# Optimization experiments

Measured on AMD Instinct MI355X. Metric: run time of the kernel, lower is better.

The kernel has to match this reference:

```python
import jax, jax.numpy as jnp
import numpy as np
from jax import lax

B, L, C = 8, 2048, 512
CR = C // 4      # SE reduction hidden
DH = C // 2      # fusion d_hidden
KS = [3, 7, 15, 20]
EPS = 1e-5


def _ln(x, g, b):
    m = jnp.mean(x, -1, keepdims=True)
    v = jnp.mean((x - m) ** 2, -1, keepdims=True)
    return (x - m) / jnp.sqrt(v + EPS) * g + b


def _bn(x, g, b, m, v):  # x: [B,C,L], eval-mode BatchNorm1d
    return (x - m[:, None]) / jnp.sqrt(v[:, None] + EPS) * g[:, None] + b[:, None]


def _forward(x, pw_w, pw_b, pw_bn_g, pw_bn_b, pw_bn_m, pw_bn_v,
             dw_w0, dw_w1, dw_w2, dw_w3, dw_b, dw_bn_g, dw_bn_b, dw_bn_m, dw_bn_v,
             se_w1, se_b1, se_w2, se_b2, se_ln_g, se_ln_b,
             df_ln_g, df_ln_b, wq, bq, wv, bv, wg, bg,
             op_w, op_b, op_ln_g, op_ln_b, fn_g, fn_b):
    Bs, Ls, Cs = x.shape
    x_in = jnp.transpose(x, (0, 2, 1))                      # [B,C,L]
    # pointwise conv (1x1) + BN + ReLU
    x_pw = jnp.einsum('oc,bcl->bol', pw_w, x_in) + pw_b[:, None]
    x_pw = jax.nn.relu(_bn(x_pw, pw_bn_g, pw_bn_b, pw_bn_m, pw_bn_v))

    enhanced = []
    for i, (w, k) in enumerate(zip([dw_w0, dw_w1, dw_w2, dw_w3], KS)):
        p = (k - 1) // 2
        y = lax.conv_general_dilated(
            x_pw, w[:, None, :], window_strides=(1,), padding=[(p, p)],
            feature_group_count=Cs, dimension_numbers=('NCH', 'OIH', 'NCH'))
        y = y + dw_b[i][:, None]
        y = jax.nn.relu(_bn(y, dw_bn_g[i], dw_bn_b[i], dw_bn_m[i], dw_bn_v[i]))
        if y.shape[2] > Ls:
            y = y[:, :, :Ls]
        elif y.shape[2] < Ls:
            y = jnp.pad(y, ((0, 0), (0, 0), (0, Ls - y.shape[2])))
        feat = jnp.transpose(y, (0, 2, 1))                  # [B,L,C]
        # ChannelAttentionBlock (SE): pool over L -> MLP -> sigmoid gate -> residual LN
        ym = jnp.mean(feat, axis=1)                          # [B,C]
        h = jax.nn.relu(ym @ se_w1[i].T + se_b1[i])          # [B,CR]
        wt = jax.nn.sigmoid(h @ se_w2[i].T + se_b2[i])       # [B,C]
        enhanced.append(_ln(feat + feat * wt[:, None, :], se_ln_g[i], se_ln_b[i]))

    # diff_conv: fixed weight w[:,:,0]=-1, w[:,:,1]=1 => every out channel is
    # sum_c(x[l+1,c]-x[l,c]); pad one zero step at the end
    s = jnp.sum(x[:, 1:] - x[:, :-1], axis=-1, keepdims=True)    # [B,L-1,1]
    diff_feat = jnp.pad(jnp.broadcast_to(s, (Bs, Ls - 1, Cs)), ((0, 0), (0, 1), (0, 0)))

    # DiffGuidedInteractiveFusion
    D = _ln(diff_feat, df_ln_g, df_ln_b)
    Q = D @ wq.T + bq                                       # [B,L,DH]
    scores = []
    for f in enhanced:
        Vi = f @ wv.T + bv                                  # [B,L,DH]
        scores.append(jnp.tanh(Q * Vi) @ wg + bg)           # [B,L]
    scores = jnp.stack(scores, axis=-1)                     # [B,L,S]
    sw = jax.nn.softmax(scores, axis=-1)
    fused = sum(sw[..., i:i + 1] * enhanced[i] for i in range(len(enhanced)))
    out = _ln(fused @ op_w.T + op_b, op_ln_g, op_ln_b)
    return _ln(out + x, fn_g, fn_b)


def setup_inputs() -> dict:
    key = jax.random.key(0)
    ks = jax.random.split(key, 12)
    r = lambda k, s: jax.random.normal(k, s, jnp.float32) * 0.02
    return {
        'x': jax.random.normal(ks[0], (B, L, C), jnp.float32),
        'pw_w': r(ks[1], (C, C)), 'pw_b': jnp.zeros(C),
        'pw_bn_g': jnp.ones(C), 'pw_bn_b': jnp.zeros(C), 'pw_bn_m': jnp.zeros(C), 'pw_bn_v': jnp.ones(C),
        'dw_w0': r(ks[2], (C, 3)), 'dw_w1': r(ks[3], (C, 7)), 'dw_w2': r(ks[4], (C, 15)), 'dw_w3': r(ks[5], (C, 20)),
        'dw_b': jnp.zeros((4, C)),
        'dw_bn_g': jnp.ones((4, C)), 'dw_bn_b': jnp.zeros((4, C)), 'dw_bn_m': jnp.zeros((4, C)), 'dw_bn_v': jnp.ones((4, C)),
        'se_w1': r(ks[6], (4, CR, C)), 'se_b1': jnp.zeros((4, CR)),
        'se_w2': r(ks[7], (4, C, CR)), 'se_b2': jnp.zeros((4, C)),
        'se_ln_g': jnp.ones((4, C)), 'se_ln_b': jnp.zeros((4, C)),
        'df_ln_g': jnp.ones(C), 'df_ln_b': jnp.zeros(C),
        'wq': r(ks[8], (DH, C)), 'bq': jnp.zeros(DH),
        'wv': r(ks[9], (DH, C)), 'bv': jnp.zeros(DH),
        'wg': r(ks[10], (DH,)), 'bg': jnp.zeros(()),
        'op_w': r(ks[11], (C, C)), 'op_b': jnp.zeros(C),
        'op_ln_g': jnp.ones(C), 'op_ln_b': jnp.zeros(C),
        'fn_g': jnp.ones(C), 'fn_b': jnp.zeros(C),
    }


def reference(x, pw_w, pw_b, pw_bn_g, pw_bn_b, pw_bn_m, pw_bn_v,
              dw_w0, dw_w1, dw_w2, dw_w3, dw_b, dw_bn_g, dw_bn_b, dw_bn_m, dw_bn_v,
              se_w1, se_b1, se_w2, se_b2, se_ln_g, se_ln_b,
              df_ln_g, df_ln_b, wq, bq, wv, bv, wg, bg,
              op_w, op_b, op_ln_g, op_ln_b, fn_g, fn_b):
    return _forward(x, pw_w, pw_b, pw_bn_g, pw_bn_b, pw_bn_m, pw_bn_v,
                    dw_w0, dw_w1, dw_w2, dw_w3, dw_b, dw_bn_g, dw_bn_b, dw_bn_m, dw_bn_v,
                    se_w1, se_b1, se_w2, se_b2, se_ln_g, se_ln_b,
                    df_ln_g, df_ln_b, wq, bq, wv, bv, wg, bg,
                    op_w, op_b, op_ln_g, op_ln_b, fn_g, fn_b)
```

## Files before the change

kernel.cpp:

```cpp
#include <hip/hip_runtime.h>
#include <math.h>

static constexpr int Bz = 8;
static constexpr int Lz = 2048;
static constexpr int Cz = 512;
static constexpr int CRz = 128;
static constexpr int DHz = 256;
static constexpr int MT = Bz * Lz;
static constexpr float EPSz = 1e-5f;

typedef unsigned short u16;
typedef __bf16 bf16x8 __attribute__((ext_vector_type(8)));
typedef float f32x4 __attribute__((ext_vector_type(4)));
typedef unsigned short u16x8 __attribute__((ext_vector_type(8)));

__device__ __forceinline__ float bf2f(u16 u) {
  unsigned int v = ((unsigned int)u) << 16;
  return __builtin_bit_cast(float, v);
}
__device__ __forceinline__ u16 f2bf(float f) {
  unsigned int b = __builtin_bit_cast(unsigned int, f);
  b += 0x7FFFu + ((b >> 16) & 1u);
  return (u16)(b >> 16);
}
__device__ __forceinline__ f32x4 mfma16(bf16x8 a, bf16x8 b, f32x4 c) {
  return __builtin_amdgcn_mfma_f32_16x16x32_bf16(a, b, c, 0, 0, 0);
}

__global__ __launch_bounds__(256) void cvt_bf16_kernel(
    const float* __restrict__ src, u16* __restrict__ dst, int n8) {
  int i = blockIdx.x * 256 + threadIdx.x;
  if (i >= n8) return;
  const float4* s = (const float4*)src;
  float4 a = s[i * 2], b = s[i * 2 + 1];
  u16x8 o;
  o[0] = f2bf(a.x); o[1] = f2bf(a.y); o[2] = f2bf(a.z); o[3] = f2bf(a.w);
  o[4] = f2bf(b.x); o[5] = f2bf(b.y); o[6] = f2bf(b.z); o[7] = f2bf(b.w);
  ((u16x8*)dst)[i] = o;
}

__global__ __launch_bounds__(256) void prep_kernel(
    const float* __restrict__ pw_b, const float* __restrict__ pw_g,
    const float* __restrict__ pw_bb, const float* __restrict__ pw_m,
    const float* __restrict__ pw_v,
    const float* __restrict__ dw_b, const float* __restrict__ dw_g,
    const float* __restrict__ dw_bb, const float* __restrict__ dw_m,
    const float* __restrict__ dw_v,
    const float* __restrict__ df_ln_b, const float* __restrict__ wq,
    const float* __restrict__ bq,
    float* __restrict__ pwA, float* __restrict__ pwB,
    float* __restrict__ dwA, float* __restrict__ dwB,
    float* __restrict__ qc) {
  const int blk = blockIdx.x;
  const int t = threadIdx.x;
  if (blk == 0) {
    for (int c = t; c < Cz; c += 256) {
      float inv = rsqrtf(pw_v[c] + EPSz);
      float a = pw_g[c] * inv;
      float bb = pw_bb[c] - pw_m[c] * a;
      pwA[c] = a;
      pwB[c] = pw_b[c] * a + bb;
    }
  } else if (blk <= 4) {
    const int i = blk - 1;
    for (int c = t; c < Cz; c += 256) {
      int idx = i * Cz + c;
      float inv = rsqrtf(dw_v[idx] + EPSz);
      float a = dw_g[idx] * inv;
      float bb = dw_bb[idx] - dw_m[idx] * a;
      dwA[idx] = a;
      dwB[idx] = dw_b[idx] * a + bb;
    }
  } else {
    if (t < DHz) {
      float s = bq[t];
      const float* w = wq + (size_t)t * Cz;
      for (int c = 0; c < Cz; c++) s += df_ln_b[c] * w[c];
      qc[t] = s;
    }
  }
}

__global__ __launch_bounds__(256, 2) void pw_mfma_kernel(
    const u16* __restrict__ Wbf, const float* __restrict__ x,
    const float* __restrict__ alpha, const float* __restrict__ beta,
    u16* __restrict__ xpw) {
  __shared__ __align__(16) char lds[74240];
  u16(*sX)[520] = (u16(*)[520])lds;
  u16(*sW)[40] = (u16(*)[40])(lds + 33280);
  u16* sC = (u16*)(lds + 33280);
  __shared__ float sAl[Cz];
  __shared__ float sBe[Cz];
  const int bat = blockIdx.x >> 6;
  const int l0 = (blockIdx.x & 63) * 32;
  const int t = threadIdx.x;
  const int lane = t & 63, w = t >> 6;
  const int fr = lane & 15, fk = (lane >> 4) * 8;
  const int mh = (w >> 1) * 16;
  const int nh = (w & 1) * 16;
#pragma unroll
  for (int rep = 0; rep < 8; rep++) {
    const int idx = rep * 256 + t;
    const int row = idx >> 6;
    const int col = (idx & 63) * 8;
    const float* src = x + ((size_t)bat * Lz + l0 + row) * Cz + col;
    float4 f0 = *(const float4*)src;
    float4 f1 = *(const float4*)(src + 4);
    u16x8 o;
    o[0] = f2bf(f0.x); o[1] = f2bf(f0.y); o[2] = f2bf(f0.z); o[3] = f2bf(f0.w);
    o[4] = f2bf(f1.x); o[5] = f2bf(f1.y); o[6] = f2bf(f1.z); o[7] = f2bf(f1.w);
    *(u16x8*)&sX[row][col] = o;
  }
  for (int c = t; c < Cz; c += 256) { sAl[c] = alpha[c]; sBe[c] = beta[c]; }
  f32x4 acc[16];
#pragma unroll
  for (int mf = 0; mf < 16; mf++)
#pragma unroll
    for (int r = 0; r < 4; r++) acc[mf][r] = 0.f;
  const int wrow = t >> 2, wch = (t & 3) * 8;
  const u16* wbase = Wbf + (size_t)wrow * Cz + wch;
  u16x8 breg[8];
#pragma unroll
  for (int rep = 0; rep < 8; rep++)
    breg[rep] = *(const u16x8*)(wbase + (size_t)rep * 64 * Cz);
  for (int k0 = 0; k0 < Cz; k0 += 32) {
    __syncthreads();
#pragma unroll
    for (int rep = 0; rep < 8; rep++)
      *(u16x8*)&sW[rep * 64 + wrow][wch] = breg[rep];
    __syncthreads();
    if (k0 + 32 < Cz) {
#pragma unroll
      for (int rep = 0; rep < 8; rep++)
        breg[rep] = *(const u16x8*)(wbase + (size_t)rep * 64 * Cz + k0 + 32);
    }
    bf16x8 bfrag = *(const bf16x8*)&sX[nh + fr][k0 + fk];
#pragma unroll
    for (int mf = 0; mf < 16; mf++) {
      bf16x8 a = *(const bf16x8*)&sW[(mh + mf) * 16 + fr][fk];
      acc[mf] = mfma16(a, bfrag, acc[mf]);
    }
  }
  __syncthreads();
#pragma unroll
  for (int mf = 0; mf < 16; mf++) {
#pragma unroll
    for (int r = 0; r < 4; r++) {
      const int o = (mh + mf) * 16 + ((lane >> 4) << 2) + r;
      const int l = nh + fr;
      float v = fmaxf(acc[mf][r] * sAl[o] + sBe[o], 0.f);
      sC[o * 40 + l] = f2bf(v);
    }
  }
  __syncthreads();
#pragma unroll
  for (int rep = 0; rep < 8; rep++) {
    const int o = rep * 64 + (t >> 2);
    const int l8 = (t & 3) * 8;
    u16x8 v = *(const u16x8*)&sC[o * 40 + l8];
    *(u16x8*)(xpw + ((size_t)(bat * Cz + o)) * Lz + l0 + l8) = v;
  }
}

template <int K>
__device__ __forceinline__ float dw_branch(const float* __restrict__ row,
                                           const float* __restrict__ wts,
                                           float a, float bb, int valid, int t,
                                           u16* __restrict__ dst) {
  constexpr int P = (K - 1) / 2;
  constexpr int W = 8 + K - 1;
  float wreg[K];
#pragma unroll
  for (int j = 0; j < K; j++) wreg[j] = wts[j];
  const int base = t * 8 - P;
  float win[W];
  if (base >= 0 && base + W <= Lz) {
#pragma unroll
    for (int j = 0; j < W; j++) {
      const int idx = base + j;
      win[j] = row[idx + (idx >> 5)];
    }
  } else {
#pragma unroll
    for (int j = 0; j < W; j++) {
      const int idx = base + j;
      win[j] = (idx >= 0 && idx < Lz) ? row[idx + (idx >> 5)] : 0.f;
    }
  }
  float acc[8] = {};
#pragma unroll
  for (int jj = 0; jj < K; jj++)
#pragma unroll
    for (int o = 0; o < 8; o++) acc[o] = fmaf(wreg[jj], win[jj + o], acc[o]);
  u16x8 ov;
  float psum = 0.f;
#pragma unroll
  for (int o = 0; o < 8; o++) {
    float v = fmaxf(acc[o] * a + bb, 0.f);
    if (t * 8 + o >= valid) v = 0.f;
    ov[o] = f2bf(v);
    psum += v;
  }
  *(u16x8*)(dst + t * 8) = ov;
  return psum;
}

__global__ __launch_bounds__(256) void dw_conv_kernel(
    const u16* __restrict__ xpw,
    const float* __restrict__ w0, const float* __restrict__ w1,
    const float* __restrict__ w2, const float* __restrict__ w3,
    const float* __restrict__ dwA, const float* __restrict__ dwB,
    u16* __restrict__ y, float* __restrict__ ysum) {
  __shared__ float row[Lz + Lz / 32];
  __shared__ float wts[48];
  __shared__ float wsum[4][4];
  const int b = blockIdx.x >> 9;
  const int c = blockIdx.x & 511;
  const int t = threadIdx.x;
  const size_t NBL = (size_t)Bz * Cz * Lz;
  {
    u16x8 v = ((const u16x8*)(xpw + ((size_t)(b * Cz + c)) * Lz))[t];
#pragma unroll
    for (int j = 0; j < 8; j++) {
      const int idx = t * 8 + j;
      row[idx + (idx >> 5)] = bf2f(v[j]);
    }
  }
  if (t < 45) {
    float wv;
    if (t < 3) wv = w0[c * 3 + t];
    else if (t < 10) wv = w1[c * 7 + (t - 3)];
    else if (t < 25) wv = w2[c * 15 + (t - 10)];
    else wv = w3[c * 20 + (t - 25)];
    wts[t] = wv;
  }
  __syncthreads();
  u16* dstb = y + ((size_t)b * Cz + c) * Lz;
  float ps[4];
  ps[0] = dw_branch<3>(row, wts + 0, dwA[c], dwB[c], Lz, t, dstb);
  ps[1] = dw_branch<7>(row, wts + 3, dwA[Cz + c], dwB[Cz + c], Lz, t,
                       dstb + NBL);
  ps[2] = dw_branch<15>(row, wts + 10, dwA[2 * Cz + c], dwB[2 * Cz + c], Lz, t,
                        dstb + 2 * NBL);
  ps[3] = dw_branch<20>(row, wts + 25, dwA[3 * Cz + c], dwB[3 * Cz + c],
                        Lz - 1, t, dstb + 3 * NBL);
#pragma unroll
  for (int off = 32; off > 0; off >>= 1) {
#pragma unroll
    for (int i = 0; i < 4; i++) ps[i] += __shfl_down(ps[i], off, 64);
  }
  if ((t & 63) == 0) {
#pragma unroll
    for (int i = 0; i < 4; i++) wsum[t >> 6][i] = ps[i];
  }
  __syncthreads();
  if (t < 4)
    ysum[(t * Bz + b) * Cz + c] =
        wsum[0][t] + wsum[1][t] + wsum[2][t] + wsum[3][t];
}

__global__ __launch_bounds__(128) void se_kernel(
    const float* __restrict__ ysum,
    const float* __restrict__ se_w1, const float* __restrict__ se_b1,
    const float* __restrict__ se_w2, const float* __restrict__ se_b2,
    float* __restrict__ sc) {
  const int i = blockIdx.x >> 3;
  const int b = blockIdx.x & 7;
  __shared__ float ym[Cz];
  __shared__ float h[CRz];
  const int t = threadIdx.x;
  const float* ys = ysum + (i * Bz + b) * Cz;
  for (int cc = t; cc < Cz; cc += 128) ym[cc] = ys[cc] * (1.f / Lz);
  __syncthreads();
  {
    const float* w1 = se_w1 + (size_t)i * CRz * Cz + (size_t)t * Cz;
    float s = se_b1[i * CRz + t];
    for (int cc = 0; cc < Cz; cc++) s += ym[cc] * w1[cc];
    h[t] = fmaxf(s, 0.f);
  }
  __syncthreads();
  for (int cc = t; cc < Cz; cc += 128) {
    const float* w2 = se_w2 + ((size_t)i * Cz + cc) * CRz;
    float s = se_b2[i * Cz + cc];
    for (int r = 0; r < CRz; r++) s += h[r] * w2[r];
    float wt = 1.f / (1.f + expf(-s));
    sc[(i * Bz + b) * Cz + cc] = 1.f + wt;
  }
}

__global__ __launch_bounds__(256) void ln_transpose_kernel(
    const u16* __restrict__ ybuf, const float* __restrict__ scv,
    const float* __restrict__ se_ln_g, const float* __restrict__ se_ln_b,
    u16* __restrict__ ebuf) {
  __shared__ u16 tile[32][522];
  __shared__ float ssc[Cz];
  const size_t NBL = (size_t)Bz * Cz * Lz;
  const int i = blockIdx.y >> 3;
  const int b = blockIdx.y & 7;
  const int l0 = blockIdx.x * 32;
  const int t = threadIdx.x;
  const u16* yb = ybuf + (size_t)i * NBL + (size_t)b * Cz * Lz;
  const float* scb = scv + (i * Bz + b) * Cz;
  for (int cc = t; cc < Cz; cc += 256) ssc[cc] = scb[cc];
#pragma unroll
  for (int rep = 0; rep < 8; rep++) {
    const int idx = rep * 256 + t;
    const int c = idx >> 2;
    const int l8 = (idx & 3) * 8;
    u16x8 v = *(const u16x8*)(yb + (size_t)c * Lz + l0 + l8);
#pragma unroll
    for (int j = 0; j < 8; j++) tile[l8 + j][c] = v[j];
  }
  __syncthreads();
  const int wave = t >> 6, lane = t & 63;
  const float* g = se_ln_g + i * Cz;
  const float* bb = se_ln_b + i * Cz;
  float sc8[8], g8[8], b8[8];
#pragma unroll
  for (int j = 0; j < 8; j++) {
    const int cc = lane + j * 64;
    sc8[j] = ssc[cc];
    g8[j] = g[cc];
    b8[j] = bb[cc];
  }
  u16* eb = ebuf + (size_t)i * NBL + ((size_t)b * Lz + l0) * Cz;
  for (int r = wave; r < 32; r += 4) {
    float vals[8];
    float s1 = 0.f, s2 = 0.f;
#pragma unroll
    for (int j = 0; j < 8; j++) {
      float v = bf2f(tile[r][lane + j * 64]) * sc8[j];
      vals[j] = v; s1 += v; s2 += v * v;
    }
    for (int off = 32; off > 0; off >>= 1) {
      s1 += __shfl_xor(s1, off, 64);
      s2 += __shfl_xor(s2, off, 64);
    }
    const float m = s1 * (1.f / Cz);
    const float var = s2 * (1.f / Cz) - m * m;
    const float inv = rsqrtf(var + EPSz);
#pragma unroll
    for (int j = 0; j < 8; j++) {
      const int cc = lane + j * 64;
      eb[(size_t)r * Cz + cc] = f2bf((vals[j] - m) * inv * g8[j] + b8[j]);
    }
  }
}

__global__ __launch_bounds__(256) void score_mfma_kernel(
    const u16* __restrict__ e0, const u16* __restrict__ e1,
    const u16* __restrict__ e2, const u16* __restrict__ e3,
    const u16* __restrict__ wvbf, const float* __restrict__ bv,
    const float* __restrict__ qc, const float* __restrict__ wg,
    const float* __restrict__ bg, float* __restrict__ scores) {
  __shared__ u16 sA[64][72];
  __shared__ u16 sB[256][72];
  __shared__ float sP[4][64];
  const int i = blockIdx.y;
  const u16* E = (i == 0) ? e0 : (i == 1) ? e1 : (i == 2) ? e2 : e3;
  const int r0 = blockIdx.x * 64;
  const int t = threadIdx.x;
  const int lane = t & 63, w = t >> 6;
  const int fr = lane & 15, fk = (lane >> 4) * 8;
  const int srow = t >> 3;
  const int kc = (t & 7) * 8;
  u16x8 areg[2], breg[8];
#pragma unroll
  for (int rep = 0; rep < 2; rep++)
    areg[rep] = *(const u16x8*)(E + (size_t)(r0 + rep * 32 + srow) * Cz + kc);
#pragma unroll
  for (int rep = 0; rep < 8; rep++)
    breg[rep] = *(const u16x8*)(wvbf + (size_t)(rep * 32 + srow) * Cz + kc);
  f32x4 acc[4][4];
#pragma unroll
  for (int m = 0; m < 4; m++)
#pragma unroll
    for (int j = 0; j < 4; j++)
#pragma unroll
      for (int r = 0; r < 4; r++) acc[m][j][r] = 0.f;
  for (int k0 = 0; k0 < Cz; k0 += 64) {
    __syncthreads();
#pragma unroll
    for (int rep = 0; rep < 2; rep++)
      *(u16x8*)&sA[rep * 32 + srow][kc] = areg[rep];
#pragma unroll
    for (int rep = 0; rep < 8; rep++)
      *(u16x8*)&sB[rep * 32 + srow][kc] = breg[rep];
    __syncthreads();
    if (k0 + 64 < Cz) {
#pragma unroll
      for (int rep = 0; rep < 2; rep++)
        areg[rep] = *(const u16x8*)(E + (size_t)(r0 + rep * 32 + srow) * Cz +
                                    k0 + 64 + kc);
#pragma unroll
      for (int rep = 0; rep < 8; rep++)
        breg[rep] = *(const u16x8*)(wvbf + (size_t)(rep * 32 + srow) * Cz +
                                    k0 + 64 + kc);
    }
#pragma unroll
    for (int ks = 0; ks < 2; ks++) {
      bf16x8 am[4], bj[4];
#pragma unroll
      for (int m = 0; m < 4; m++)
        am[m] = *(const bf16x8*)&sA[m * 16 + fr][ks * 32 + fk];
#pragma unroll
      for (int j = 0; j < 4; j++)
        bj[j] = *(const bf16x8*)&sB[(w * 4 + j) * 16 + fr][ks * 32 + fk];
#pragma unroll
      for (int m = 0; m < 4; m++)
#pragma unroll
        for (int j = 0; j < 4; j++)
          acc[m][j] = mfma16(am[m], bj[j], acc[m][j]);
    }
  }
  float part[4][4];
#pragma unroll
  for (int m = 0; m < 4; m++)
#pragma unroll
    for (int r = 0; r < 4; r++) part[m][r] = 0.f;
#pragma unroll
  for (int j = 0; j < 4; j++) {
    const int dh = (w * 4 + j) * 16 + fr;
    const float bvn = bv[dh], qcn = qc[dh], wgn = wg[dh];
#pragma unroll
    for (int m = 0; m < 4; m++)
#pragma unroll
      for (int r = 0; r < 4; r++)
        part[m][r] += tanhf(qcn * (acc[m][j][r] + bvn)) * wgn;
  }
#pragma unroll
  for (int off = 1; off < 16; off <<= 1) {
#pragma unroll
    for (int m = 0; m < 4; m++)
#pragma unroll
      for (int r = 0; r < 4; r++)
        part[m][r] += __shfl_xor(part[m][r], off, 64);
  }
  if (fr == 0) {
#pragma unroll
    for (int m = 0; m < 4; m++)
#pragma unroll
      for (int r = 0; r < 4; r++)
        sP[w][m * 16 + ((lane >> 4) << 2) + r] = part[m][r];
  }
  __syncthreads();
  if (t < 64) {
    float s = sP[0][t] + sP[1][t] + sP[2][t] + sP[3][t] + bg[0];
    scores[(size_t)i * MT + r0 + t] = s;
  }
}

__global__ __launch_bounds__(256, 2) void op_mfma_kernel(
    const u16* __restrict__ e0, const u16* __restrict__ e1,
    const u16* __restrict__ e2, const u16* __restrict__ e3,
    const float* __restrict__ scores, const u16* __restrict__ opwbf,
    const float* __restrict__ opb,
    const float* __restrict__ g1, const float* __restrict__ b1,
    const float* __restrict__ x,
    const float* __restrict__ g2, const float* __restrict__ b2,
    float* __restrict__ out) {
  __shared__ u16 sA[32][520];
  __shared__ u16 sB[512][40];
  __shared__ float sw4[4][32];
  const int m0 = blockIdx.x * 32;
  const int t = threadIdx.x;
  const int lane = t & 63, w = t >> 6;
  const int fr = lane & 15, fk = (lane >> 4) * 8;
  const int mh = (w >> 1) * 16;
  const int nh = (w & 1) * 16;
  if (t < 32) {
    const int r = m0 + t;
    float s0 = scores[r], s1 = scores[MT + r], s2 = scores[2 * MT + r],
          s3 = scores[3 * MT + r];
    float mx = fmaxf(fmaxf(s0, s1), fmaxf(s2, s3));
    float x0 = expf(s0 - mx), x1 = expf(s1 - mx), x2 = expf(s2 - mx),
          x3 = expf(s3 - mx);
    float inv = 1.f / (x0 + x1 + x2 + x3);
    sw4[0][t] = x0 * inv; sw4[1][t] = x1 * inv;
    sw4[2][t] = x2 * inv; sw4[3][t] = x3 * inv;
  }
  __syncthreads();
#pragma unroll
  for (int rep = 0; rep < 8; rep++) {
    const int idx = rep * 256 + t;
    const int row = idx >> 6;
    const int col = (idx & 63) * 8;
    const size_t off = (size_t)(m0 + row) * Cz + col;
    u16x8 v0 = *(const u16x8*)(e0 + off);
    u16x8 v1 = *(const u16x8*)(e1 + off);
    u16x8 v2 = *(const u16x8*)(e2 + off);
    u16x8 v3 = *(const u16x8*)(e3 + off);
    const float x0 = sw4[0][row], x1 = sw4[1][row], x2 = sw4[2][row],
                x3 = sw4[3][row];
    u16x8 o;
#pragma unroll
    for (int j = 0; j < 8; j++)
      o[j] = f2bf(x0 * bf2f(v0[j]) + x1 * bf2f(v1[j]) + x2 * bf2f(v2[j]) +
                  x3 * bf2f(v3[j]));
    *(u16x8*)&sA[row][col] = o;
  }
  f32x4 acc[16];
#pragma unroll
  for (int nf = 0; nf < 16; nf++)
#pragma unroll
    for (int r = 0; r < 4; r++) acc[nf][r] = 0.f;
  const int wrow = t >> 2, wch = (t & 3) * 8;
  const u16* wbase = opwbf + (size_t)wrow * Cz + wch;
  u16x8 breg[8];
#pragma unroll
  for (int rep = 0; rep < 8; rep++)
    breg[rep] = *(const u16x8*)(wbase + (size_t)rep * 64 * Cz);
  for (int k0 = 0; k0 < Cz; k0 += 32) {
    __syncthreads();
#pragma unroll
    for (int rep = 0; rep < 8; rep++)
      *(u16x8*)&sB[rep * 64 + wrow][wch] = breg[rep];
    __syncthreads();
    if (k0 + 32 < Cz) {
#pragma unroll
      for (int rep = 0; rep < 8; rep++)
        breg[rep] = *(const u16x8*)(wbase + (size_t)rep * 64 * Cz + k0 + 32);
    }
    bf16x8 a = *(const bf16x8*)&sA[mh + fr][k0 + fk];
#pragma unroll
    for (int nf = 0; nf < 16; nf++) {
      bf16x8 b = *(const bf16x8*)&sB[(nh + nf) * 16 + fr][fk];
      acc[nf] = mfma16(a, b, acc[nf]);
    }
  }
  __syncthreads();
  u16* sC = (u16*)&sA[0][0];
#pragma unroll
  for (int nf = 0; nf < 16; nf++) {
    const int n = (nh + nf) * 16 + fr;
    const float ob = opb[n];
#pragma unroll
    for (int r = 0; r < 4; r++) {
      const int row = mh + ((lane >> 4) << 2) + r;
      sC[row * 520 + n] = f2bf(acc[nf][r] + ob);
    }
  }
  __syncthreads();
  float g1v[8], b1v[8], g2v[8], b2v[8];
  {
    float4 a0 = ((const float4*)g1)[lane * 2], a1 = ((const float4*)g1)[lane * 2 + 1];
    float4 c0 = ((const float4*)b1)[lane * 2], c1 = ((const float4*)b1)[lane * 2 + 1];
    float4 d0 = ((const float4*)g2)[lane * 2], d1 = ((const float4*)g2)[lane * 2 + 1];
    float4 e0v = ((const float4*)b2)[lane * 2], e1v = ((const float4*)b2)[lane * 2 + 1];
    g1v[0]=a0.x; g1v[1]=a0.y; g1v[2]=a0.z; g1v[3]=a0.w;
    g1v[4]=a1.x; g1v[5]=a1.y; g1v[6]=a1.z; g1v[7]=a1.w;
    b1v[0]=c0.x; b1v[1]=c0.y; b1v[2]=c0.z; b1v[3]=c0.w;
    b1v[4]=c1.x; b1v[5]=c1.y; b1v[6]=c1.z; b1v[7]=c1.w;
    g2v[0]=d0.x; g2v[1]=d0.y; g2v[2]=d0.z; g2v[3]=d0.w;
    g2v[4]=d1.x; g2v[5]=d1.y; g2v[6]=d1.z; g2v[7]=d1.w;
    b2v[0]=e0v.x; b2v[1]=e0v.y; b2v[2]=e0v.z; b2v[3]=e0v.w;
    b2v[4]=e1v.x; b2v[5]=e1v.y; b2v[6]=e1v.z; b2v[7]=e1v.w;
  }
  for (int rr = 0; rr < 8; rr++) {
    const int row = w * 8 + rr;
    u16x8 av = *(const u16x8*)&sC[row * 520 + lane * 8];
    float v[8];
    float s1 = 0.f, s2 = 0.f;
#pragma unroll
    for (int j = 0; j < 8; j++) {
      v[j] = bf2f(av[j]);
      s1 += v[j]; s2 += v[j] * v[j];
    }
    for (int off = 1; off < 64; off <<= 1) {
      s1 += __shfl_xor(s1, off, 64);
      s2 += __shfl_xor(s2, off, 64);
    }
    const float m1 = s1 * (1.f / Cz);
    const float iv1 = rsqrtf(s2 * (1.f / Cz) - m1 * m1 + EPSz);
    const float* xr = x + (size_t)(m0 + row) * Cz;
    float4 xa = ((const float4*)xr)[lane * 2], xb = ((const float4*)xr)[lane * 2 + 1];
    float xv[8] = {xa.x, xa.y, xa.z, xa.w, xb.x, xb.y, xb.z, xb.w};
    float tv[8];
    s1 = 0.f; s2 = 0.f;
#pragma unroll
    for (int j = 0; j < 8; j++) {
      tv[j] = (v[j] - m1) * iv1 * g1v[j] + b1v[j] + xv[j];
      s1 += tv[j]; s2 += tv[j] * tv[j];
    }
    for (int off = 1; off < 64; off <<= 1) {
      s1 += __shfl_xor(s1, off, 64);
      s2 += __shfl_xor(s2, off, 64);
    }
    const float m2 = s1 * (1.f / Cz);
    const float iv2 = rsqrtf(s2 * (1.f / Cz) - m2 * m2 + EPSz);
    float4 oa, ob;
    oa.x = (tv[0] - m2) * iv2 * g2v[0] + b2v[0];
    oa.y = (tv[1] - m2) * iv2 * g2v[1] + b2v[1];
    oa.z = (tv[2] - m2) * iv2 * g2v[2] + b2v[2];
    oa.w = (tv[3] - m2) * iv2 * g2v[3] + b2v[3];
    ob.x = (tv[4] - m2) * iv2 * g2v[4] + b2v[4];
    ob.y = (tv[5] - m2) * iv2 * g2v[5] + b2v[5];
    ob.z = (tv[6] - m2) * iv2 * g2v[6] + b2v[6];
    ob.w = (tv[7] - m2) * iv2 * g2v[7] + b2v[7];
    float* orow = out + (size_t)(m0 + row) * Cz;
    ((float4*)orow)[lane * 2] = oa;
    ((float4*)orow)[lane * 2 + 1] = ob;
  }
}

extern "C" void kernel_launch(void* const* d_in, const int* in_sizes, int n_in,
                              void* d_out, int out_size, void* d_ws,
                              size_t ws_size, hipStream_t stream) {
  const float* x = (const float*)d_in[0];
  const float* pw_w = (const float*)d_in[1];
  const float* pw_b = (const float*)d_in[2];
  const float* pw_bn_g = (const float*)d_in[3];
  const float* pw_bn_b = (const float*)d_in[4];
  const float* pw_bn_m = (const float*)d_in[5];
  const float* pw_bn_v = (const float*)d_in[6];
  const float* dw_w0 = (const float*)d_in[7];
  const float* dw_w1 = (const float*)d_in[8];
  const float* dw_w2 = (const float*)d_in[9];
  const float* dw_w3 = (const float*)d_in[10];
  const float* dw_b = (const float*)d_in[11];
  const float* dw_bn_g = (const float*)d_in[12];
  const float* dw_bn_b = (const float*)d_in[13];
  const float* dw_bn_m = (const float*)d_in[14];
  const float* dw_bn_v = (const float*)d_in[15];
  const float* se_w1 = (const float*)d_in[16];
  const float* se_b1 = (const float*)d_in[17];
  const float* se_w2 = (const float*)d_in[18];
  const float* se_b2 = (const float*)d_in[19];
  const float* se_ln_g = (const float*)d_in[20];
  const float* se_ln_b = (const float*)d_in[21];
  const float* df_ln_b = (const float*)d_in[23];
  const float* wq = (const float*)d_in[24];
  const float* bq = (const float*)d_in[25];
  const float* wv = (const float*)d_in[26];
  const float* bv = (const float*)d_in[27];
  const float* wg = (const float*)d_in[28];
  const float* bg = (const float*)d_in[29];
  const float* op_w = (const float*)d_in[30];
  const float* op_b = (const float*)d_in[31];
  const float* op_ln_g = (const float*)d_in[32];
  const float* op_ln_b = (const float*)d_in[33];
  const float* fn_g = (const float*)d_in[34];
  const float* fn_b = (const float*)d_in[35];
  float* out = (float*)d_out;

  const size_t NBL = (size_t)Bz * Cz * Lz;
  char* p = (char*)d_ws;
  p += NBL * 2;
  u16* xpw = (u16*)p; p += NBL * 2;
  u16* ybuf = (u16*)p; p += 4 * NBL * 2;
  u16* ebuf = (u16*)p; p += 4 * NBL * 2;
  u16* pwwbf = (u16*)p; p += (size_t)Cz * Cz * 2;
  u16* wvbf = (u16*)p; p += (size_t)DHz * Cz * 2;
  u16* opwbf = (u16*)p; p += (size_t)Cz * Cz * 2;
  float* fbuf = (float*)p;
  float* ysum = fbuf;
  float* scv = fbuf + 16384;
  float* scores = fbuf + 32768;
  float* pwA = fbuf + 98304;
  float* pwB = pwA + 512;
  float* dwA = pwB + 512;
  float* dwB = dwA + 2048;
  float* qc = dwB + 2048;

  cvt_bf16_kernel<<<Cz * Cz / 8 / 256, 256, 0, stream>>>(pw_w, pwwbf,
                                                         Cz * Cz / 8);
  cvt_bf16_kernel<<<DHz * Cz / 8 / 256, 256, 0, stream>>>(wv, wvbf,
                                                          DHz * Cz / 8);
  cvt_bf16_kernel<<<Cz * Cz / 8 / 256, 256, 0, stream>>>(op_w, opwbf,
                                                         Cz * Cz / 8);

  prep_kernel<<<6, 256, 0, stream>>>(pw_b, pw_bn_g, pw_bn_b, pw_bn_m, pw_bn_v,
                                     dw_b, dw_bn_g, dw_bn_b, dw_bn_m, dw_bn_v,
                                     df_ln_b, wq, bq, pwA, pwB, dwA, dwB, qc);

  pw_mfma_kernel<<<Bz * (Lz / 32), 256, 0, stream>>>(pwwbf, x, pwA, pwB, xpw);

  dw_conv_kernel<<<Bz * Cz, 256, 0, stream>>>(xpw, dw_w0, dw_w1, dw_w2, dw_w3,
                                              dwA, dwB, ybuf, ysum);

  se_kernel<<<32, 128, 0, stream>>>(ysum, se_w1, se_b1, se_w2, se_b2, scv);

  ln_transpose_kernel<<<dim3(Lz / 32, 4 * Bz), 256, 0, stream>>>(
      ybuf, scv, se_ln_g, se_ln_b, ebuf);

  score_mfma_kernel<<<dim3(MT / 64, 4), 256, 0, stream>>>(
      ebuf, ebuf + NBL, ebuf + 2 * NBL, ebuf + 3 * NBL, wvbf, bv, qc, wg, bg,
      scores);

  op_mfma_kernel<<<MT / 32, 256, 0, stream>>>(
      ebuf, ebuf + NBL, ebuf + 2 * NBL, ebuf + 3 * NBL, scores, opwbf, op_b,
      op_ln_g, op_ln_b, x, fn_g, fn_b, out);
}
```

Measured before the change: 211.7 us.

## Load GEMM activation operands into registers, shrink LDS, merge prep launches

The pointwise-conv and output-projection GEMM kernels stop staging the 32-row activation tile in shared memory. Each lane now loads and converts its own MFMA fragment straight into registers, half of K at a time. This shrinks LDS per block so launch bounds can be raised to 3 blocks per CU. The three weight-conversion kernels and the prep kernel are also merged into one launch. The cost is more register pressure and uncoalesced per-lane global loads of the activation rows.

```diff
diff --git a/kernel.cpp b/kernel.cpp
--- a/kernel.cpp
+++ b/kernel.cpp
@@ -23,23 +23,17 @@
   b += 0x7FFFu + ((b >> 16) & 1u);
   return (u16)(b >> 16);
 }
+__device__ __forceinline__ bf16x8 as_bf(u16x8 v) {
+  return __builtin_bit_cast(bf16x8, v);
+}
 __device__ __forceinline__ f32x4 mfma16(bf16x8 a, bf16x8 b, f32x4 c) {
   return __builtin_amdgcn_mfma_f32_16x16x32_bf16(a, b, c, 0, 0, 0);
 }
 
-__global__ __launch_bounds__(256) void cvt_bf16_kernel(
-    const float* __restrict__ src, u16* __restrict__ dst, int n8) {
-  int i = blockIdx.x * 256 + threadIdx.x;
-  if (i >= n8) return;
-  const float4* s = (const float4*)src;
-  float4 a = s[i * 2], b = s[i * 2 + 1];
-  u16x8 o;
-  o[0] = f2bf(a.x); o[1] = f2bf(a.y); o[2] = f2bf(a.z); o[3] = f2bf(a.w);
-  o[4] = f2bf(b.x); o[5] = f2bf(b.y); o[6] = f2bf(b.z); o[7] = f2bf(b.w);
-  ((u16x8*)dst)[i] = o;
-}
-
-__global__ __launch_bounds__(256) void prep_kernel(
+__global__ __launch_bounds__(256) void prep_cvt_kernel(
+    const float* __restrict__ pw_w, const float* __restrict__ wv,
+    const float* __restrict__ op_w,
+    u16* __restrict__ pwwbf, u16* __restrict__ wvbf, u16* __restrict__ opwbf,
     const float* __restrict__ pw_b, const float* __restrict__ pw_g,
     const float* __restrict__ pw_bb, const float* __restrict__ pw_m,
     const float* __restrict__ pw_v,
@@ -53,7 +47,24 @@
     float* __restrict__ qc) {
   const int blk = blockIdx.x;
   const int t = threadIdx.x;
-  if (blk == 0) {
+  if (blk < 320) {
+    const float* src;
+    u16* dst;
+    int i;
+    if (blk < 128) { src = pw_w; dst = pwwbf; i = blk; }
+    else if (blk < 192) { src = wv; dst = wvbf; i = blk - 128; }
+    else { src = op_w; dst = opwbf; i = blk - 192; }
+    const int idx = i * 256 + t;
+    const float4* s = (const float4*)src;
+    float4 a = s[idx * 2], b = s[idx * 2 + 1];
+    u16x8 o;
+    o[0] = f2bf(a.x); o[1] = f2bf(a.y); o[2] = f2bf(a.z); o[3] = f2bf(a.w);
+    o[4] = f2bf(b.x); o[5] = f2bf(b.y); o[6] = f2bf(b.z); o[7] = f2bf(b.w);
+    ((u16x8*)dst)[idx] = o;
+    return;
+  }
+  const int sec = blk - 320;
+  if (sec == 0) {
     for (int c = t; c < Cz; c += 256) {
       float inv = rsqrtf(pw_v[c] + EPSz);
       float a = pw_g[c] * inv;
@@ -61,8 +72,8 @@
       pwA[c] = a;
       pwB[c] = pw_b[c] * a + bb;
     }
-  } else if (blk <= 4) {
-    const int i = blk - 1;
+  } else if (sec <= 4) {
+    const int i = sec - 1;
     for (int c = t; c < Cz; c += 256) {
       int idx = i * Cz + c;
       float inv = rsqrtf(dw_v[idx] + EPSz);
@@ -81,14 +92,13 @@
   }
 }
 
-__global__ __launch_bounds__(256, 2) void pw_mfma_kernel(
+__global__ __launch_bounds__(256, 3) void pw_mfma_kernel(
     const u16* __restrict__ Wbf, const float* __restrict__ x,
     const float* __restrict__ alpha, const float* __restrict__ beta,
     u16* __restrict__ xpw) {
-  __shared__ __align__(16) char lds[74240];
-  u16(*sX)[520] = (u16(*)[520])lds;
-  u16(*sW)[40] = (u16(*)[40])(lds + 33280);
-  u16* sC = (u16*)(lds + 33280);
+  __shared__ __align__(16) char lds[40960];
+  u16(*sW)[40] = (u16(*)[40])lds;
+  u16* sC = (u16*)lds;
   __shared__ float sAl[Cz];
   __shared__ float sBe[Cz];
   const int bat = blockIdx.x >> 6;
@@ -98,19 +108,6 @@
   const int fr = lane & 15, fk = (lane >> 4) * 8;
   const int mh = (w >> 1) * 16;
   const int nh = (w & 1) * 16;
-#pragma unroll
-  for (int rep = 0; rep < 8; rep++) {
-    const int idx = rep * 256 + t;
-    const int row = idx >> 6;
-    const int col = (idx & 63) * 8;
-    const float* src = x + ((size_t)bat * Lz + l0 + row) * Cz + col;
-    float4 f0 = *(const float4*)src;
-    float4 f1 = *(const float4*)(src + 4);
-    u16x8 o;
-    o[0] = f2bf(f0.x); o[1] = f2bf(f0.y); o[2] = f2bf(f0.z); o[3] = f2bf(f0.w);
-    o[4] = f2bf(f1.x); o[5] = f2bf(f1.y); o[6] = f2bf(f1.z); o[7] = f2bf(f1.w);
-    *(u16x8*)&sX[row][col] = o;
-  }
   for (int c = t; c < Cz; c += 256) { sAl[c] = alpha[c]; sBe[c] = beta[c]; }
   f32x4 acc[16];
 #pragma unroll
@@ -123,22 +120,37 @@
 #pragma unroll
   for (int rep = 0; rep < 8; rep++)
     breg[rep] = *(const u16x8*)(wbase + (size_t)rep * 64 * Cz);
-  for (int k0 = 0; k0 < Cz; k0 += 32) {
-    __syncthreads();
-#pragma unroll
-    for (int rep = 0; rep < 8; rep++)
-      *(u16x8*)&sW[rep * 64 + wrow][wch] = breg[rep];
-    __syncthreads();
-    if (k0 + 32 < Cz) {
+  const float* xrow = x + ((size_t)bat * Lz + l0 + nh + fr) * Cz;
+  for (int half = 0; half < 2; half++) {
+    bf16x8 xreg[8];
+#pragma unroll
+    for (int ks = 0; ks < 8; ks++) {
+      const int col = half * 256 + ks * 32 + fk;
+      float4 f0 = *(const float4*)(xrow + col);
+      float4 f1 = *(const float4*)(xrow + col + 4);
+      u16x8 o;
+      o[0] = f2bf(f0.x); o[1] = f2bf(f0.y); o[2] = f2bf(f0.z); o[3] = f2bf(f0.w);
+      o[4] = f2bf(f1.x); o[5] = f2bf(f1.y); o[6] = f2bf(f1.z); o[7] = f2bf(f1.w);
+      xreg[ks] = as_bf(o);
+    }
+    for (int ks = 0; ks < 8; ks++) {
+      const int gk = half * 8 + ks;
+      __syncthreads();
 #pragma unroll
       for (int rep = 0; rep < 8; rep++)
-        breg[rep] = *(const u16x8*)(wbase + (size_t)rep * 64 * Cz + k0 + 32);
-    }
-    bf16x8 bfrag = *(const bf16x8*)&sX[nh + fr][k0 + fk];
-#pragma unroll
-    for (int mf = 0; mf < 16; mf++) {
-      bf16x8 a = *(const bf16x8*)&sW[(mh + mf) * 16 + fr][fk];
-      acc[mf] = mfma16(a, bfrag, acc[mf]);
+        *(u16x8*)&sW[rep * 64 + wrow][wch] = breg[rep];
+      __syncthreads();
+      if (gk < 15) {
+#pragma unroll
+        for (int rep = 0; rep < 8; rep++)
+          breg[rep] = *(const u16x8*)(wbase + (size_t)rep * 64 * Cz +
+                                      (gk + 1) * 32);
+      }
+#pragma unroll
+      for (int mf = 0; mf < 16; mf++) {
+        bf16x8 a = *(const bf16x8*)&sW[(mh + mf) * 16 + fr][fk];
+        acc[mf] = mfma16(a, xreg[ks], acc[mf]);
+      }
     }
   }
   __syncthreads();
@@ -450,7 +462,7 @@
   }
 }
 
-__global__ __launch_bounds__(256, 2) void op_mfma_kernel(
+__global__ __launch_bounds__(256, 3) void op_mfma_kernel(
     const u16* __restrict__ e0, const u16* __restrict__ e1,
     const u16* __restrict__ e2, const u16* __restrict__ e3,
     const float* __restrict__ scores, const u16* __restrict__ opwbf,
@@ -459,8 +471,9 @@
     const float* __restrict__ x,
     const float* __restrict__ g2, const float* __restrict__ b2,
     float* __restrict__ out) {
-  __shared__ u16 sA[32][520];
-  __shared__ u16 sB[512][40];
+  __shared__ __align__(16) char lds[40960];
+  u16(*sB)[40] = (u16(*)[40])lds;
+  u16* sC = (u16*)lds;
   __shared__ float sw4[4][32];
   const int m0 = blockIdx.x * 32;
   const int t = threadIdx.x;
@@ -480,25 +493,13 @@
     sw4[2][t] = x2 * inv; sw4[3][t] = x3 * inv;
   }
   __syncthreads();
-#pragma unroll
-  for (int rep = 0; rep < 8; rep++) {
-    const int idx = rep * 256 + t;
-    const int row = idx >> 6;
-    const int col = (idx & 63) * 8;
-    const size_t off = (size_t)(m0 + row) * Cz + col;
-    u16x8 v0 = *(const u16x8*)(e0 + off);
-    u16x8 v1 = *(const u16x8*)(e1 + off);
-    u16x8 v2 = *(const u16x8*)(e2 + off);
-    u16x8 v3 = *(const u16x8*)(e3 + off);
-    const float x0 = sw4[0][row], x1 = sw4[1][row], x2 = sw4[2][row],
-                x3 = sw4[3][row];
-    u16x8 o;
-#pragma unroll
-    for (int j = 0; j < 8; j++)
-      o[j] = f2bf(x0 * bf2f(v0[j]) + x1 * bf2f(v1[j]) + x2 * bf2f(v2[j]) +
-                  x3 * bf2f(v3[j]));
-    *(u16x8*)&sA[row][col] = o;
-  }
+  const float sw0 = sw4[0][mh + fr], sw1 = sw4[1][mh + fr],
+              sw2 = sw4[2][mh + fr], sw3 = sw4[3][mh + fr];
+  const size_t arow = (size_t)(m0 + mh + fr) * Cz;
+  const u16* e0r = e0 + arow;
+  const u16* e1r = e1 + arow;
+  const u16* e2r = e2 + arow;
+  const u16* e3r = e3 + arow;
   f32x4 acc[16];
 #pragma unroll
   for (int nf = 0; nf < 16; nf++)
@@ -510,26 +511,43 @@
 #pragma unroll
   for (int rep = 0; rep < 8; rep++)
     breg[rep] = *(const u16x8*)(wbase + (size_t)rep * 64 * Cz);
-  for (int k0 = 0; k0 < Cz; k0 += 32) {
-    __syncthreads();
-#pragma unroll
-    for (int rep = 0; rep < 8; rep++)
-      *(u16x8*)&sB[rep * 64 + wrow][wch] = breg[rep];
-    __syncthreads();
-    if (k0 + 32 < Cz) {
+  for (int half = 0; half < 2; half++) {
+    bf16x8 areg[8];
+#pragma unroll
+    for (int ks = 0; ks < 8; ks++) {
+      const int col = half * 256 + ks * 32 + fk;
+      u16x8 v0 = *(const u16x8*)(e0r + col);
+      u16x8 v1 = *(const u16x8*)(e1r + col);
+      u16x8 v2 = *(const u16x8*)(e2r + col);
+      u16x8 v3 = *(const u16x8*)(e3r + col);
+      u16x8 o;
+#pragma unroll
+      for (int j = 0; j < 8; j++)
+        o[j] = f2bf(sw0 * bf2f(v0[j]) + sw1 * bf2f(v1[j]) +
+                    sw2 * bf2f(v2[j]) + sw3 * bf2f(v3[j]));
+      areg[ks] = as_bf(o);
+    }
+    for (int ks = 0; ks < 8; ks++) {
+      const int gk = half * 8 + ks;
+      __syncthreads();
 #pragma unroll
       for (int rep = 0; rep < 8; rep++)
-        breg[rep] = *(const u16x8*)(wbase + (size_t)rep * 64 * Cz + k0 + 32);
-    }
-    bf16x8 a = *(const bf16x8*)&sA[mh + fr][k0 + fk];
-#pragma unroll
-    for (int nf = 0; nf < 16; nf++) {
-      bf16x8 b = *(const bf16x8*)&sB[(nh + nf) * 16 + fr][fk];
-      acc[nf] = mfma16(a, b, acc[nf]);
-    }
-  }
-  __syncthreads();
-  u16* sC = (u16*)&sA[0][0];
+        *(u16x8*)&sB[rep * 64 + wrow][wch] = breg[rep];
+      __syncthreads();
+      if (gk < 15) {
+#pragma unroll
+        for (int rep = 0; rep < 8; rep++)
+          breg[rep] = *(const u16x8*)(wbase + (size_t)rep * 64 * Cz +
+                                      (gk + 1) * 32);
+      }
+#pragma unroll
+      for (int nf = 0; nf < 16; nf++) {
+        bf16x8 b = *(const bf16x8*)&sB[(nh + nf) * 16 + fr][fk];
+        acc[nf] = mfma16(areg[ks], b, acc[nf]);
+      }
+    }
+  }
+  __syncthreads();
 #pragma unroll
   for (int nf = 0; nf < 16; nf++) {
     const int n = (nh + nf) * 16 + fr;
@@ -662,16 +680,10 @@
   float* dwB = dwA + 2048;
   float* qc = dwB + 2048;
 
-  cvt_bf16_kernel<<<Cz * Cz / 8 / 256, 256, 0, stream>>>(pw_w, pwwbf,
-                                                         Cz * Cz / 8);
-  cvt_bf16_kernel<<<DHz * Cz / 8 / 256, 256, 0, stream>>>(wv, wvbf,
-                                                          DHz * Cz / 8);
-  cvt_bf16_kernel<<<Cz * Cz / 8 / 256, 256, 0, stream>>>(op_w, opwbf,
-                                                         Cz * Cz / 8);
-
-  prep_kernel<<<6, 256, 0, stream>>>(pw_b, pw_bn_g, pw_bn_b, pw_bn_m, pw_bn_v,
-                                     dw_b, dw_bn_g, dw_bn_b, dw_bn_m, dw_bn_v,
-                                     df_ln_b, wq, bq, pwA, pwB, dwA, dwB, qc);
+  prep_cvt_kernel<<<326, 256, 0, stream>>>(
+      pw_w, wv, op_w, pwwbf, wvbf, opwbf, pw_b, pw_bn_g, pw_bn_b, pw_bn_m,
+      pw_bn_v, dw_b, dw_bn_g, dw_bn_b, dw_bn_m, dw_bn_v, df_ln_b, wq, bq, pwA,
+      pwB, dwA, dwB, qc);
 
   pw_mfma_kernel<<<Bz * (Lz / 32), 256, 0, stream>>>(pwwbf, x, pwA, pwB, xpw);
 
```

Result: slower. 246.6 us (+16.5%).

## Load GEMM weight fragments directly from global memory instead of staging through LDS

Applied to the files above, without the earlier changes.

In the pointwise-conv and output-projection MFMA kernels, the per-k-step LDS staging of the 512x32 weight slice (with two barriers per step) is removed. Each wave now reads its weight fragments straight from global memory, relying on L2/cache hits since every block shares the same weight. This shrinks LDS use, so launch bounds are raised to three blocks per CU. The trade is more, less coalesced global loads per MFMA with no software prefetch, in exchange for fewer barriers and higher occupancy.

```diff
diff --git a/kernel.cpp b/kernel.cpp
--- a/kernel.cpp
+++ b/kernel.cpp
@@ -81,16 +81,13 @@
   }
 }
 
-__global__ __launch_bounds__(256, 2) void pw_mfma_kernel(
+__global__ __launch_bounds__(256, 3) void pw_mfma_kernel(
     const u16* __restrict__ Wbf, const float* __restrict__ x,
     const float* __restrict__ alpha, const float* __restrict__ beta,
     u16* __restrict__ xpw) {
-  __shared__ __align__(16) char lds[74240];
+  __shared__ __align__(16) char lds[40960];
   u16(*sX)[520] = (u16(*)[520])lds;
-  u16(*sW)[40] = (u16(*)[40])(lds + 33280);
-  u16* sC = (u16*)(lds + 33280);
-  __shared__ float sAl[Cz];
-  __shared__ float sBe[Cz];
+  u16* sC = (u16*)lds;
   const int bat = blockIdx.x >> 6;
   const int l0 = (blockIdx.x & 63) * 32;
   const int t = threadIdx.x;
@@ -111,33 +108,18 @@
     o[4] = f2bf(f1.x); o[5] = f2bf(f1.y); o[6] = f2bf(f1.z); o[7] = f2bf(f1.w);
     *(u16x8*)&sX[row][col] = o;
   }
-  for (int c = t; c < Cz; c += 256) { sAl[c] = alpha[c]; sBe[c] = beta[c]; }
+  __syncthreads();
   f32x4 acc[16];
 #pragma unroll
   for (int mf = 0; mf < 16; mf++)
 #pragma unroll
     for (int r = 0; r < 4; r++) acc[mf][r] = 0.f;
-  const int wrow = t >> 2, wch = (t & 3) * 8;
-  const u16* wbase = Wbf + (size_t)wrow * Cz + wch;
-  u16x8 breg[8];
-#pragma unroll
-  for (int rep = 0; rep < 8; rep++)
-    breg[rep] = *(const u16x8*)(wbase + (size_t)rep * 64 * Cz);
+  const u16* aptr = Wbf + (size_t)(mh * 16 + fr) * Cz + fk;
   for (int k0 = 0; k0 < Cz; k0 += 32) {
-    __syncthreads();
-#pragma unroll
-    for (int rep = 0; rep < 8; rep++)
-      *(u16x8*)&sW[rep * 64 + wrow][wch] = breg[rep];
-    __syncthreads();
-    if (k0 + 32 < Cz) {
-#pragma unroll
-      for (int rep = 0; rep < 8; rep++)
-        breg[rep] = *(const u16x8*)(wbase + (size_t)rep * 64 * Cz + k0 + 32);
-    }
     bf16x8 bfrag = *(const bf16x8*)&sX[nh + fr][k0 + fk];
 #pragma unroll
     for (int mf = 0; mf < 16; mf++) {
-      bf16x8 a = *(const bf16x8*)&sW[(mh + mf) * 16 + fr][fk];
+      bf16x8 a = *(const bf16x8*)(aptr + (size_t)mf * 16 * Cz + k0);
       acc[mf] = mfma16(a, bfrag, acc[mf]);
     }
   }
@@ -148,7 +130,7 @@
     for (int r = 0; r < 4; r++) {
       const int o = (mh + mf) * 16 + ((lane >> 4) << 2) + r;
       const int l = nh + fr;
-      float v = fmaxf(acc[mf][r] * sAl[o] + sBe[o], 0.f);
+      float v = fmaxf(acc[mf][r] * alpha[o] + beta[o], 0.f);
       sC[o * 40 + l] = f2bf(v);
     }
   }
@@ -450,7 +432,7 @@
   }
 }
 
-__global__ __launch_bounds__(256, 2) void op_mfma_kernel(
+__global__ __launch_bounds__(256, 3) void op_mfma_kernel(
     const u16* __restrict__ e0, const u16* __restrict__ e1,
     const u16* __restrict__ e2, const u16* __restrict__ e3,
     const float* __restrict__ scores, const u16* __restrict__ opwbf,
@@ -460,7 +442,6 @@
     const float* __restrict__ g2, const float* __restrict__ b2,
     float* __restrict__ out) {
   __shared__ u16 sA[32][520];
-  __shared__ u16 sB[512][40];
   __shared__ float sw4[4][32];
   const int m0 = blockIdx.x * 32;
   const int t = threadIdx.x;
@@ -499,32 +480,18 @@
                   x3 * bf2f(v3[j]));
     *(u16x8*)&sA[row][col] = o;
   }
+  __syncthreads();
   f32x4 acc[16];
 #pragma unroll
   for (int nf = 0; nf < 16; nf++)
 #pragma unroll
     for (int r = 0; r < 4; r++) acc[nf][r] = 0.f;
-  const int wrow = t >> 2, wch = (t & 3) * 8;
-  const u16* wbase = opwbf + (size_t)wrow * Cz + wch;
-  u16x8 breg[8];
-#pragma unroll
-  for (int rep = 0; rep < 8; rep++)
-    breg[rep] = *(const u16x8*)(wbase + (size_t)rep * 64 * Cz);
+  const u16* bptr = opwbf + (size_t)(nh * 16 + fr) * Cz + fk;
   for (int k0 = 0; k0 < Cz; k0 += 32) {
-    __syncthreads();
-#pragma unroll
-    for (int rep = 0; rep < 8; rep++)
-      *(u16x8*)&sB[rep * 64 + wrow][wch] = breg[rep];
-    __syncthreads();
-    if (k0 + 32 < Cz) {
-#pragma unroll
-      for (int rep = 0; rep < 8; rep++)
-        breg[rep] = *(const u16x8*)(wbase + (size_t)rep * 64 * Cz + k0 + 32);
-    }
     bf16x8 a = *(const bf16x8*)&sA[mh + fr][k0 + fk];
 #pragma unroll
     for (int nf = 0; nf < 16; nf++) {
-      bf16x8 b = *(const bf16x8*)&sB[(nh + nf) * 16 + fr][fk];
+      bf16x8 b = *(const bf16x8*)(bptr + (size_t)nf * 16 * Cz + k0);
       acc[nf] = mfma16(a, b, acc[nf]);
     }
   }
```

Measured after the change: 300.6 us. 1.42x slower.

## Hold activation fragments in registers to shrink LDS and raise GEMM occupancy

Applied to the files above, without the earlier changes.

In the pointwise and output-projection GEMM kernels, the 32-row activation tile is staged through LDS in two halves and each wave's fragments are kept in registers (16 bf16x8). The full activation tile then no longer needs to stay resident in LDS, and one buffer is reused for the weight slices and the epilogue. LDS per block drops to about 41 KB, and launch bounds are raised from 2 to 3 blocks per CU to improve latency hiding. The cost is extra register pressure (64 more VGPRs per thread alongside 64 accumulator registers) under a tighter register budget, plus added barriers during staging.

```diff
diff --git a/kernel.cpp b/kernel.cpp
--- a/kernel.cpp
+++ b/kernel.cpp
@@ -81,14 +81,11 @@
   }
 }
 
-__global__ __launch_bounds__(256, 2) void pw_mfma_kernel(
+__global__ __launch_bounds__(256, 3) void pw_mfma_kernel(
     const u16* __restrict__ Wbf, const float* __restrict__ x,
     const float* __restrict__ alpha, const float* __restrict__ beta,
     u16* __restrict__ xpw) {
-  __shared__ __align__(16) char lds[74240];
-  u16(*sX)[520] = (u16(*)[520])lds;
-  u16(*sW)[40] = (u16(*)[40])(lds + 33280);
-  u16* sC = (u16*)(lds + 33280);
+  __shared__ __align__(16) u16 lds[512 * 40];
   __shared__ float sAl[Cz];
   __shared__ float sBe[Cz];
   const int bat = blockIdx.x >> 6;
@@ -98,20 +95,30 @@
   const int fr = lane & 15, fk = (lane >> 4) * 8;
   const int mh = (w >> 1) * 16;
   const int nh = (w & 1) * 16;
-#pragma unroll
-  for (int rep = 0; rep < 8; rep++) {
-    const int idx = rep * 256 + t;
-    const int row = idx >> 6;
-    const int col = (idx & 63) * 8;
-    const float* src = x + ((size_t)bat * Lz + l0 + row) * Cz + col;
-    float4 f0 = *(const float4*)src;
-    float4 f1 = *(const float4*)(src + 4);
-    u16x8 o;
-    o[0] = f2bf(f0.x); o[1] = f2bf(f0.y); o[2] = f2bf(f0.z); o[3] = f2bf(f0.w);
-    o[4] = f2bf(f1.x); o[5] = f2bf(f1.y); o[6] = f2bf(f1.z); o[7] = f2bf(f1.w);
-    *(u16x8*)&sX[row][col] = o;
-  }
   for (int c = t; c < Cz; c += 256) { sAl[c] = alpha[c]; sBe[c] = beta[c]; }
+  bf16x8 xregs[16];
+  for (int half = 0; half < 2; half++) {
+#pragma unroll
+    for (int rep = 0; rep < 4; rep++) {
+      const int idx = rep * 256 + t;
+      const int row = idx >> 5;
+      const int ch = idx & 31;
+      const float* src =
+          x + ((size_t)bat * Lz + l0 + row) * Cz + half * 256 + ch * 8;
+      float4 f0 = *(const float4*)src;
+      float4 f1 = *(const float4*)(src + 4);
+      u16x8 o;
+      o[0] = f2bf(f0.x); o[1] = f2bf(f0.y); o[2] = f2bf(f0.z); o[3] = f2bf(f0.w);
+      o[4] = f2bf(f1.x); o[5] = f2bf(f1.y); o[6] = f2bf(f1.z); o[7] = f2bf(f1.w);
+      *(u16x8*)&lds[row * 256 + ch * 8] = o;
+    }
+    __syncthreads();
+#pragma unroll
+    for (int ks = 0; ks < 8; ks++)
+      xregs[half * 8 + ks] =
+          *(const bf16x8*)&lds[(nh + fr) * 256 + ks * 32 + fk];
+    __syncthreads();
+  }
   f32x4 acc[16];
 #pragma unroll
   for (int mf = 0; mf < 16; mf++)
@@ -127,21 +134,22 @@
     __syncthreads();
 #pragma unroll
     for (int rep = 0; rep < 8; rep++)
-      *(u16x8*)&sW[rep * 64 + wrow][wch] = breg[rep];
+      *(u16x8*)&lds[(rep * 64 + wrow) * 40 + wch] = breg[rep];
     __syncthreads();
     if (k0 + 32 < Cz) {
 #pragma unroll
       for (int rep = 0; rep < 8; rep++)
         breg[rep] = *(const u16x8*)(wbase + (size_t)rep * 64 * Cz + k0 + 32);
     }
-    bf16x8 bfrag = *(const bf16x8*)&sX[nh + fr][k0 + fk];
+    bf16x8 bfrag = xregs[k0 >> 5];
 #pragma unroll
     for (int mf = 0; mf < 16; mf++) {
-      bf16x8 a = *(const bf16x8*)&sW[(mh + mf) * 16 + fr][fk];
+      bf16x8 a = *(const bf16x8*)&lds[((mh + mf) * 16 + fr) * 40 + fk];
       acc[mf] = mfma16(a, bfrag, acc[mf]);
     }
   }
   __syncthreads();
+  u16* sC = lds;
 #pragma unroll
   for (int mf = 0; mf < 16; mf++) {
 #pragma unroll
@@ -450,7 +458,7 @@
   }
 }
 
-__global__ __launch_bounds__(256, 2) void op_mfma_kernel(
+__global__ __launch_bounds__(256, 3) void op_mfma_kernel(
     const u16* __restrict__ e0, const u16* __restrict__ e1,
     const u16* __restrict__ e2, const u16* __restrict__ e3,
     const float* __restrict__ scores, const u16* __restrict__ opwbf,
@@ -459,8 +467,7 @@
     const float* __restrict__ x,
     const float* __restrict__ g2, const float* __restrict__ b2,
     float* __restrict__ out) {
-  __shared__ u16 sA[32][520];
-  __shared__ u16 sB[512][40];
+  __shared__ __align__(16) u16 lds[512 * 40];
   __shared__ float sw4[4][32];
   const int m0 = blockIdx.x * 32;
   const int t = threadIdx.x;
@@ -480,24 +487,33 @@
     sw4[2][t] = x2 * inv; sw4[3][t] = x3 * inv;
   }
   __syncthreads();
-#pragma unroll
-  for (int rep = 0; rep < 8; rep++) {
-    const int idx = rep * 256 + t;
-    const int row = idx >> 6;
-    const int col = (idx & 63) * 8;
-    const size_t off = (size_t)(m0 + row) * Cz + col;
-    u16x8 v0 = *(const u16x8*)(e0 + off);
-    u16x8 v1 = *(const u16x8*)(e1 + off);
-    u16x8 v2 = *(const u16x8*)(e2 + off);
-    u16x8 v3 = *(const u16x8*)(e3 + off);
-    const float x0 = sw4[0][row], x1 = sw4[1][row], x2 = sw4[2][row],
-                x3 = sw4[3][row];
-    u16x8 o;
-#pragma unroll
-    for (int j = 0; j < 8; j++)
-      o[j] = f2bf(x0 * bf2f(v0[j]) + x1 * bf2f(v1[j]) + x2 * bf2f(v2[j]) +
-                  x3 * bf2f(v3[j]));
-    *(u16x8*)&sA[row][col] = o;
+  bf16x8 aregs[16];
+  for (int half = 0; half < 2; half++) {
+#pragma unroll
+    for (int rep = 0; rep < 4; rep++) {
+      const int idx = rep * 256 + t;
+      const int row = idx >> 5;
+      const int ch = idx & 31;
+      const size_t off = (size_t)(m0 + row) * Cz + half * 256 + ch * 8;
+      u16x8 v0 = *(const u16x8*)(e0 + off);
+      u16x8 v1 = *(const u16x8*)(e1 + off);
+      u16x8 v2 = *(const u16x8*)(e2 + off);
+      u16x8 v3 = *(const u16x8*)(e3 + off);
+      const float x0 = sw4[0][row], x1 = sw4[1][row], x2 = sw4[2][row],
+                  x3 = sw4[3][row];
+      u16x8 o;
+#pragma unroll
+      for (int j = 0; j < 8; j++)
+        o[j] = f2bf(x0 * bf2f(v0[j]) + x1 * bf2f(v1[j]) + x2 * bf2f(v2[j]) +
+                    x3 * bf2f(v3[j]));
+      *(u16x8*)&lds[row * 256 + ch * 8] = o;
+    }
+    __syncthreads();
+#pragma unroll
+    for (int ks = 0; ks < 8; ks++)
+      aregs[half * 8 + ks] =
+          *(const bf16x8*)&lds[(mh + fr) * 256 + ks * 32 + fk];
+    __syncthreads();
   }
   f32x4 acc[16];
 #pragma unroll
@@ -514,22 +530,22 @@
     __syncthreads();
 #pragma unroll
     for (int rep = 0; rep < 8; rep++)
-      *(u16x8*)&sB[rep * 64 + wrow][wch] = breg[rep];
+      *(u16x8*)&lds[(rep * 64 + wrow) * 40 + wch] = breg[rep];
     __syncthreads();
     if (k0 + 32 < Cz) {
 #pragma unroll
       for (int rep = 0; rep < 8; rep++)
         breg[rep] = *(const u16x8*)(wbase + (size_t)rep * 64 * Cz + k0 + 32);
     }
-    bf16x8 a = *(const bf16x8*)&sA[mh + fr][k0 + fk];
+    bf16x8 a = aregs[k0 >> 5];
 #pragma unroll
     for (int nf = 0; nf < 16; nf++) {
-      bf16x8 b = *(const bf16x8*)&sB[(nh + nf) * 16 + fr][fk];
+      bf16x8 b = *(const bf16x8*)&lds[((nh + nf) * 16 + fr) * 40 + fk];
       acc[nf] = mfma16(a, b, acc[nf]);
     }
   }
   __syncthreads();
-  u16* sC = (u16*)&sA[0][0];
+  u16* sC = lds;
 #pragma unroll
   for (int nf = 0; nf < 16; nf++) {
     const int n = (nh + nf) * 16 + fr;
```

Result: slower. 229.4 us (+8.4%).
